# Performance work log

Measured on AMD Instinct MI355X. Metric: run time of the kernel, lower is better.

Reference implementation:

```python
import jax, jax.numpy as jnp
import numpy as np

# Standard SMPL kinematic tree (24 joints)
PARENTS = np.array([-1, 0, 0, 0, 1, 2, 3, 4, 5, 6, 7, 8, 9, 9, 9, 12, 13, 14, 16, 17, 18, 19, 20, 21], dtype=np.int32)
B, V, J, NB = 1024, 6890, 24, 10  # batch, vertices, joints, betas


def _rodrigues(r):
    """Axis-angle (..., 3) -> rotation matrices (..., 3, 3)."""
    theta = jnp.sqrt(jnp.sum(r * r, axis=-1, keepdims=True) + 1e-8)
    axis = r / theta
    c = jnp.cos(theta)[..., None]
    s = jnp.sin(theta)[..., None]
    x, y, z = axis[..., 0], axis[..., 1], axis[..., 2]
    zeros = jnp.zeros_like(x)
    K = jnp.stack([zeros, -z, y, z, zeros, -x, -y, x, zeros], axis=-1).reshape(r.shape[:-1] + (3, 3))
    outer = axis[..., :, None] * axis[..., None, :]
    eye = jnp.eye(3, dtype=r.dtype)
    return c * eye + (1.0 - c) * outer + s * K


def setup_inputs() -> dict:
    key = jax.random.key(0)
    ks = jax.random.split(key, 9)
    shape = jax.random.normal(ks[0], (B, NB), dtype=jnp.float32)
    body_pose = jax.random.normal(ks[1], (B, J - 1, 3), dtype=jnp.float32) * 0.2
    pelvis_rotation = jax.random.normal(ks[2], (B, 3), dtype=jnp.float32) * 0.2
    global_translation = jax.random.normal(ks[3], (B, 3), dtype=jnp.float32)
    v_template = jax.random.normal(ks[4], (V, 3), dtype=jnp.float32) * 0.3
    shapedirs = jax.random.normal(ks[5], (V, 3, NB), dtype=jnp.float32) * 0.01
    posedirs = jax.random.normal(ks[6], ((J - 1) * 9, V * 3), dtype=jnp.float32) * 0.01
    lbs_weights = jax.nn.softmax(jax.random.normal(ks[7], (V, J), dtype=jnp.float32) * 4.0, axis=-1)
    J_regressor = jax.nn.softmax(jax.random.normal(ks[8], (J, V), dtype=jnp.float32) * 4.0, axis=-1)
    parents = jnp.asarray(PARENTS)
    return {"shape": shape, "body_pose": body_pose, "pelvis_rotation": pelvis_rotation,
            "global_translation": global_translation, "v_template": v_template,
            "shapedirs": shapedirs, "posedirs": posedirs, "lbs_weights": lbs_weights,
            "J_regressor": J_regressor, "parents": parents}


def reference(shape, body_pose, pelvis_rotation, global_translation,
              v_template, shapedirs, posedirs, lbs_weights, J_regressor, parents):
    b = shape.shape[0]
    dtype = shape.dtype
    # --- shape blendshapes ---
    v_shaped = v_template + jnp.einsum('bl,vcl->bvc', shape, shapedirs)        # (B, V, 3)
    joints = jnp.einsum('jv,bvc->bjc', J_regressor, v_shaped)                  # (B, J, 3)
    # --- pose rotations + pose blendshapes ---
    full_pose = jnp.concatenate([pelvis_rotation[:, None, :], body_pose], axis=1)  # (B, J, 3)
    rot = _rodrigues(full_pose)                                                # (B, J, 3, 3)
    pose_feat = (rot[:, 1:] - jnp.eye(3, dtype=dtype)).reshape(b, (J - 1) * 9)
    v_posed = v_shaped + (pose_feat @ posedirs).reshape(b, -1, 3)              # (B, V, 3)
    # --- forward kinematics along tree ---
    rel_joints = joints.at[:, 1:].add(-joints[:, PARENTS[1:]])                 # (B, J, 3)
    T = jnp.concatenate([rot, rel_joints[..., None]], axis=-1)                 # (B, J, 3, 4)
    bottom = jnp.broadcast_to(jnp.asarray([0, 0, 0, 1], dtype=dtype), (b, J, 1, 4))
    T = jnp.concatenate([T, bottom], axis=-2)                                  # (B, J, 4, 4)
    chain = [T[:, 0]]
    for j in range(1, J):
        chain.append(chain[int(PARENTS[j])] @ T[:, j])
    A = jnp.stack(chain, axis=1)                                               # (B, J, 4, 4)
    # --- remove rest-pose joint locations ---
    t_corr = A[..., :3, 3] - jnp.einsum('bjxy,bjy->bjx', A[..., :3, :3], joints)
    A_rel = A.at[..., :3, 3].set(t_corr)
    # --- linear blend skinning ---
    Tv = jnp.einsum('vj,bjxy->bvxy', lbs_weights, A_rel)                       # (B, V, 4, 4)
    verts = jnp.einsum('bvxy,bvy->bvx', Tv[..., :3, :3], v_posed) + Tv[..., :3, 3]
    return verts + global_translation[:, None, :]                              # (B, V, 3)
```

## Files before the change

kernel.cpp:

```cpp
#include <hip/hip_runtime.h>
#include <stdint.h>

#define V_   6890
#define N3   20670
#define NPAD 20736
#define VPAD 7168
#define J_   24
#define NB_  10
#define KP   207
#define KE   224
#define LDP  201

typedef __attribute__((ext_vector_type(8))) short bf16x8;
typedef __attribute__((ext_vector_type(4))) float f32x4;

__device__ __forceinline__ float bf2f(ushort u) {
    union { uint32_t u; float f; } cv; cv.u = ((uint32_t)u) << 16; return cv.f;
}
__device__ __forceinline__ ushort f2bf(float f) {
    union { float f; uint32_t u; } cv; cv.f = f;
    uint32_t u = cv.u;
    u += 0x7FFFu + ((u >> 16) & 1u);
    return (ushort)(u >> 16);
}

__global__ __launch_bounds__(256) void k_jreg(const float* __restrict__ jreg,
                                              const float* __restrict__ vt,
                                              const float* __restrict__ sd,
                                              float* __restrict__ jsp) {
    int j = blockIdx.x, c = blockIdx.y;
    int t = threadIdx.x;
    float acc[33];
#pragma unroll
    for (int i = 0; i < 33; i++) acc[i] = 0.f;
#pragma unroll
    for (int it = 0; it < 2; it++) {
        int v = c * 512 + it * 256 + t;
        if (v < V_) {
            float w = jreg[(size_t)j * V_ + v];
            acc[0] += w * vt[v * 3 + 0];
            acc[1] += w * vt[v * 3 + 1];
            acc[2] += w * vt[v * 3 + 2];
            const float* sdv = sd + (size_t)v * 30;
#pragma unroll
            for (int i = 0; i < 30; i++) acc[3 + i] += w * sdv[i];
        }
    }
    __shared__ float red[256][33];
#pragma unroll
    for (int i = 0; i < 33; i++) red[t][i] = acc[i];
    __syncthreads();
    for (int s = 128; s > 0; s >>= 1) {
        if (t < s) {
#pragma unroll
            for (int i = 0; i < 33; i++) red[t][i] += red[t + s][i];
        }
        __syncthreads();
    }
    if (t < 33) jsp[(size_t)(j * 14 + c) * 33 + t] = red[0][t];
}

__global__ __launch_bounds__(832) void k_jred(const float* __restrict__ jsp,
                                              float* __restrict__ js) {
    int t = threadIdx.x;
    if (t >= 792) return;
    int j = t / 33, i = t % 33;
    float s = 0.f;
#pragma unroll
    for (int c = 0; c < 14; c++) s += jsp[(size_t)(j * 14 + c) * 33 + i];
    js[t] = s;
}

__global__ __launch_bounds__(256) void k_bext(const float* __restrict__ pd,
                                              const float* __restrict__ sd,
                                              const float* __restrict__ vt,
                                              ushort* __restrict__ bt) {
    int n  = blockIdx.x * 256 + threadIdx.x;
    int k0 = blockIdx.y * 8;
    bool valid = n < N3;
    union { ushort s[8]; uint4 v; } u;
#pragma unroll
    for (int i = 0; i < 8; i++) {
        int k = k0 + i;
        float x = 0.f;
        if (valid) {
            if (k < KP)              x = pd[(size_t)k * N3 + n];
            else if (k < KP + NB_)   x = sd[(size_t)n * NB_ + (k - KP)];
            else if (k == KP + NB_)  x = vt[n];
        }
        u.s[i] = f2bf(x);
    }
    *(uint4*)(bt + (size_t)n * KE + k0) = u.v;
}

__global__ __launch_bounds__(256) void k_wbf(const float* __restrict__ lw,
                                             ushort* __restrict__ w_hi,
                                             ushort* __restrict__ w_lo) {
    int i = blockIdx.x * 256 + threadIdx.x;
    int v = i >> 5, j = i & 31;
    float x = (j < 24 && v < V_) ? lw[(size_t)v * 24 + j] : 0.f;
    ushort hi = f2bf(x);
    w_hi[i] = hi;
    w_lo[i] = f2bf(x - bf2f(hi));
}

__global__ __launch_bounds__(64) void k_pose(const float* __restrict__ shape,
                                             const float* __restrict__ body_pose,
                                             const float* __restrict__ pelvis,
                                             const float* __restrict__ js,
                                             ushort* __restrict__ pfext,
                                             ushort* __restrict__ aT_hi,
                                             ushort* __restrict__ aT_lo,
                                             int Breal) {
    int b = blockIdx.x;
    int t = threadIdx.x;
    if (b >= Breal) {
        uint32_t* pz = (uint32_t*)(pfext + (size_t)b * KE);
        for (int i = t; i < KE / 2; i += 64) pz[i] = 0;
        return;
    }
    __shared__ float Rs[24][9];
    __shared__ float Js[24][3];
    __shared__ float As[24][12];

    if (t < 24) {
        float rx, ry, rz;
        if (t == 0) {
            rx = pelvis[b * 3 + 0]; ry = pelvis[b * 3 + 1]; rz = pelvis[b * 3 + 2];
        } else {
            const float* p = body_pose + ((size_t)b * 23 + (t - 1)) * 3;
            rx = p[0]; ry = p[1]; rz = p[2];
        }
        float th = sqrtf(rx * rx + ry * ry + rz * rz + 1e-8f);
        float inv = 1.f / th;
        float x = rx * inv, y = ry * inv, z = rz * inv;
        float c = cosf(th), s = sinf(th), omc = 1.f - c;
        float R[9];
        R[0] = c + omc * x * x;     R[1] = omc * x * y - s * z; R[2] = omc * x * z + s * y;
        R[3] = omc * y * x + s * z; R[4] = c + omc * y * y;     R[5] = omc * y * z - s * x;
        R[6] = omc * z * x - s * y; R[7] = omc * z * y + s * x; R[8] = c + omc * z * z;
#pragma unroll
        for (int e = 0; e < 9; e++) Rs[t][e] = R[e];

        const float* jsj = js + t * 33;
        float sh[10];
#pragma unroll
        for (int l = 0; l < 10; l++) sh[l] = shape[b * 10 + l];
#pragma unroll
        for (int c2 = 0; c2 < 3; c2++) {
            float a = jsj[c2];
#pragma unroll
            for (int l = 0; l < 10; l++) a += sh[l] * jsj[3 + c2 * 10 + l];
            Js[t][c2] = a;
        }
        ushort* pf = pfext + (size_t)b * KE;
        if (t >= 1) {
#pragma unroll
            for (int e = 0; e < 9; e++) {
                float v = R[e] - ((e == 0 || e == 4 || e == 8) ? 1.f : 0.f);
                pf[(t - 1) * 9 + e] = f2bf(v);
            }
        } else {
            for (int l = 0; l < 10; l++) pf[KP + l] = f2bf(sh[l]);
            pf[KP + NB_] = 0x3F80;
            for (int k = KP + NB_ + 1; k < KE; k++) pf[k] = 0;
        }
    }
    __syncthreads();

    if (t < 12) {
        int row = t >> 2, col = t & 3;
        As[0][t] = (col < 3) ? Rs[0][row * 3 + col] : Js[0][row];
    }
    __syncthreads();
    const int par[24] = {-1,0,0,0,1,2,3,4,5,6,7,8,9,9,9,12,13,14,16,17,18,19,20,21};
#pragma unroll 1
    for (int j = 1; j < 24; j++) {
        int p = par[j];
        float val = 0.f;
        if (t < 12) {
            int row = t >> 2, col = t & 3;
            if (col < 3) {
                val = As[p][row * 4 + 0] * Rs[j][0 * 3 + col]
                    + As[p][row * 4 + 1] * Rs[j][1 * 3 + col]
                    + As[p][row * 4 + 2] * Rs[j][2 * 3 + col];
            } else {
                float relx = Js[j][0] - Js[p][0];
                float rely = Js[j][1] - Js[p][1];
                float relz = Js[j][2] - Js[p][2];
                val = As[p][row * 4 + 0] * relx + As[p][row * 4 + 1] * rely
                    + As[p][row * 4 + 2] * relz + As[p][row * 4 + 3];
            }
        }
        __syncthreads();
        if (t < 12) As[j][t] = val;
        __syncthreads();
    }
    if (t < 24) {
        float tc[3];
#pragma unroll
        for (int row = 0; row < 3; row++) {
            float r0 = As[t][row * 4 + 0], r1 = As[t][row * 4 + 1], r2 = As[t][row * 4 + 2];
            tc[row] = As[t][row * 4 + 3] - (r0 * Js[t][0] + r1 * Js[t][1] + r2 * Js[t][2]);
        }
        As[t][3] = tc[0]; As[t][7] = tc[1]; As[t][11] = tc[2];
    }
    __syncthreads();
    ushort* dh = aT_hi + (size_t)b * 512;
    ushort* dl = aT_lo + (size_t)b * 512;
    for (int i = t; i < 512; i += 64) {
        int e = i >> 5, j = i & 31;
        float val = (e < 12 && j < 24) ? As[j][e] : 0.f;
        ushort hi = f2bf(val);
        dh[i] = hi;
        dl[i] = f2bf(val - bf2f(hi));
    }
}

__global__ __launch_bounds__(256) void k_fused(const ushort* __restrict__ bt,
                                               const ushort* __restrict__ pfext,
                                               const ushort* __restrict__ aT_hi,
                                               const ushort* __restrict__ aT_lo,
                                               const ushort* __restrict__ w_hi,
                                               const ushort* __restrict__ w_lo,
                                               const float* __restrict__ trans,
                                               float* __restrict__ vert,
                                               int Breal) {
    int lane = threadIdx.x & 63;
    int wv   = threadIdx.x >> 6;
    int quad = lane >> 4;
    int m    = lane & 15;
    int vtile = blockIdx.x;
    int nbase = vtile * 192;
    int bbase = blockIdx.y * 64 + wv * 16;

    __shared__ float posed[64][LDP];

    f32x4 acc[12];
#pragma unroll
    for (int f = 0; f < 12; f++) acc[f] = (f32x4){0.f, 0.f, 0.f, 0.f};

    const ushort* bp = pfext + (size_t)(bbase + m) * KE + quad * 8;
    const ushort* ap = bt + (size_t)(nbase + m) * KE + quad * 8;
#pragma unroll 2
    for (int ks = 0; ks < 7; ks++) {
        bf16x8 bfrag = *(const bf16x8*)(bp + ks * 32);
#pragma unroll
        for (int f = 0; f < 12; f++) {
            bf16x8 afrag = *(const bf16x8*)(ap + (size_t)(f * 16) * KE + ks * 32);
            acc[f] = __builtin_amdgcn_mfma_f32_16x16x32_bf16(afrag, bfrag, acc[f], 0, 0, 0);
        }
    }
    {
        float* dst0 = &posed[wv * 16 + m][quad * 4];
#pragma unroll
        for (int f = 0; f < 12; f++) {
            float* dst = dst0 + f * 16;
            dst[0] = acc[f][0]; dst[1] = acc[f][1]; dst[2] = acc[f][2]; dst[3] = acc[f][3];
        }
    }
    __syncthreads();

    bf16x8 Wh[4], Wl[4];
#pragma unroll
    for (int i = 0; i < 4; i++) {
        size_t offw = (size_t)((vtile * 4 + i) * 16 + m) * 32 + quad * 8;
        Wh[i] = *(const bf16x8*)(w_hi + offw);
        Wl[i] = *(const bf16x8*)(w_lo + offw);
    }

#pragma unroll 1
    for (int bb = 0; bb < 16; bb++) {
        int b = bbase + bb;
        if (b >= Breal) break;
        size_t aoff = (size_t)b * 512 + m * 32 + quad * 8;
        bf16x8 Ah = *(const bf16x8*)(aT_hi + aoff);
        bf16x8 Al = *(const bf16x8*)(aT_lo + aoff);
        float tq = (quad < 3) ? trans[b * 3 + quad] : 0.f;
        const float* pr = &posed[wv * 16 + bb][0];
        float* vrow = vert + (size_t)b * N3;
#pragma unroll
        for (int i = 0; i < 4; i++) {
            int vloc = i * 16 + m;
            int v = vtile * 64 + vloc;
            float p0 = pr[vloc * 3 + 0];
            float p1 = pr[vloc * 3 + 1];
            float p2 = pr[vloc * 3 + 2];
            f32x4 a2 = (f32x4){0.f, 0.f, 0.f, 0.f};
            a2 = __builtin_amdgcn_mfma_f32_16x16x32_bf16(Ah, Wh[i], a2, 0, 0, 0);
            a2 = __builtin_amdgcn_mfma_f32_16x16x32_bf16(Al, Wh[i], a2, 0, 0, 0);
            a2 = __builtin_amdgcn_mfma_f32_16x16x32_bf16(Ah, Wl[i], a2, 0, 0, 0);
            float res = a2[0] * p0 + a2[1] * p1 + a2[2] * p2 + a2[3] + tq;
            if (quad < 3 && v < V_)
                vrow[3 * v + quad] = res;
        }
    }
}

extern "C" void kernel_launch(void* const* d_in, const int* in_sizes, int n_in,
                              void* d_out, int out_size, void* d_ws, size_t ws_size,
                              hipStream_t stream) {
    const float* shape = (const float*)d_in[0];
    const float* bpose = (const float*)d_in[1];
    const float* pelv  = (const float*)d_in[2];
    const float* trans = (const float*)d_in[3];
    const float* vt    = (const float*)d_in[4];
    const float* sd    = (const float*)d_in[5];
    const float* pd    = (const float*)d_in[6];
    const float* lw    = (const float*)d_in[7];
    const float* jr    = (const float*)d_in[8];
    float* out = (float*)d_out;

    int B    = in_sizes[0] / NB_;
    int Bpad = (B + 63) & ~63;

    char* ws = (char*)d_ws;
    size_t off = 0;
    auto alloc = [&](size_t bytes) { char* p = ws + off; off += (bytes + 255) & ~(size_t)255; return p; };
    float*  jsp   = (float*) alloc(24 * 14 * 33 * 4);
    float*  js    = (float*) alloc(24 * 33 * 4);
    ushort* pfext = (ushort*)alloc((size_t)Bpad * KE * 2);
    ushort* aT_hi = (ushort*)alloc((size_t)B * 512 * 2);
    ushort* aT_lo = (ushort*)alloc((size_t)B * 512 * 2);
    ushort* w_hi  = (ushort*)alloc((size_t)VPAD * 32 * 2);
    ushort* w_lo  = (ushort*)alloc((size_t)VPAD * 32 * 2);
    ushort* bt    = (ushort*)alloc((size_t)NPAD * KE * 2);

    k_jreg<<<dim3(24, 14), 256, 0, stream>>>(jr, vt, sd, jsp);
    k_jred<<<1, 832, 0, stream>>>(jsp, js);
    k_bext<<<dim3(NPAD / 256, KE / 8), 256, 0, stream>>>(pd, sd, vt, bt);
    k_wbf<<<VPAD * 32 / 256, 256, 0, stream>>>(lw, w_hi, w_lo);
    k_pose<<<Bpad, 64, 0, stream>>>(shape, bpose, pelv, js, pfext, aT_hi, aT_lo, B);
    k_fused<<<dim3(NPAD / 192, Bpad / 64), 256, 0, stream>>>(bt, pfext, aT_hi, aT_lo,
                                                             w_hi, w_lo, trans, out, B);
}
```

Measured before the change: 217.1 us.

## Retile fused skinning kernel to 32-batch blocks with XCD swizzle and prefetch

The fused GEMM+skinning kernel now uses a 1D grid of 32-batch by 192-column tiles. The four waves split into two batch halves by two column halves, so each wave only reads the posed values it wrote, which replaces __syncthreads with an LDS waitcnt. A block-index swizzle spreads consecutive tiles across the 8 XCDs, the per-batch transform fragments are prefetched one iteration ahead, and the LDS row pitch is padded to allow aligned vector stores. The change doubles the number of blocks and halves accumulator registers, at the cost of loading pfext rows twice as often per column tile.

```diff
diff --git a/kernel.cpp b/kernel.cpp
--- a/kernel.cpp
+++ b/kernel.cpp
@@ -9,7 +9,7 @@
 #define NB_  10
 #define KP   207
 #define KE   224
-#define LDP  201
+#define LDP  204
 
 typedef __attribute__((ext_vector_type(8))) short bf16x8;
 typedef __attribute__((ext_vector_type(4))) float f32x4;
@@ -225,67 +225,78 @@
                                                const ushort* __restrict__ w_lo,
                                                const float* __restrict__ trans,
                                                float* __restrict__ vert,
-                                               int Breal) {
+                                               int Breal, int NY) {
     int lane = threadIdx.x & 63;
     int wv   = threadIdx.x >> 6;
     int quad = lane >> 4;
     int m    = lane & 15;
-    int vtile = blockIdx.x;
-    int nbase = vtile * 192;
-    int bbase = blockIdx.y * 64 + wv * 16;
-
-    __shared__ float posed[64][LDP];
-
-    f32x4 acc[12];
-#pragma unroll
-    for (int f = 0; f < 12; f++) acc[f] = (f32x4){0.f, 0.f, 0.f, 0.f};
-
-    const ushort* bp = pfext + (size_t)(bbase + m) * KE + quad * 8;
-    const ushort* ap = bt + (size_t)(nbase + m) * KE + quad * 8;
+    int bh   = wv & 1;
+    int nh   = wv >> 1;
+
+    int bid = blockIdx.x;
+    int cpx = (108 * NY) >> 3;
+    int sw  = (bid & 7) * cpx + (bid >> 3);
+    unsigned uNY = (unsigned)NY;
+    int vtile = (int)((unsigned)sw / uNY);
+    int by    = sw - vtile * NY;
+
+    int nbase_w = vtile * 192 + nh * 96;
+    int bbase_w = by * 32 + bh * 16;
+
+    __shared__ __align__(16) float posed[32][LDP];
+
+    bf16x8 Wh[2], Wl[2];
+#pragma unroll
+    for (int i = 0; i < 2; i++) {
+        size_t offw = (size_t)((vtile * 4 + nh * 2 + i) * 16 + m) * 32 + quad * 8;
+        Wh[i] = *(const bf16x8*)(w_hi + offw);
+        Wl[i] = *(const bf16x8*)(w_lo + offw);
+    }
+
+    f32x4 acc[6];
+#pragma unroll
+    for (int f = 0; f < 6; f++) acc[f] = (f32x4){0.f, 0.f, 0.f, 0.f};
+
+    const ushort* bp = pfext + (size_t)(bbase_w + m) * KE + quad * 8;
+    const ushort* ap = bt + (size_t)(nbase_w + m) * KE + quad * 8;
 #pragma unroll 2
     for (int ks = 0; ks < 7; ks++) {
         bf16x8 bfrag = *(const bf16x8*)(bp + ks * 32);
 #pragma unroll
-        for (int f = 0; f < 12; f++) {
+        for (int f = 0; f < 6; f++) {
             bf16x8 afrag = *(const bf16x8*)(ap + (size_t)(f * 16) * KE + ks * 32);
             acc[f] = __builtin_amdgcn_mfma_f32_16x16x32_bf16(afrag, bfrag, acc[f], 0, 0, 0);
         }
     }
-    {
-        float* dst0 = &posed[wv * 16 + m][quad * 4];
-#pragma unroll
-        for (int f = 0; f < 12; f++) {
-            float* dst = dst0 + f * 16;
-            dst[0] = acc[f][0]; dst[1] = acc[f][1]; dst[2] = acc[f][2]; dst[3] = acc[f][3];
-        }
-    }
-    __syncthreads();
-
-    bf16x8 Wh[4], Wl[4];
-#pragma unroll
-    for (int i = 0; i < 4; i++) {
-        size_t offw = (size_t)((vtile * 4 + i) * 16 + m) * 32 + quad * 8;
-        Wh[i] = *(const bf16x8*)(w_hi + offw);
-        Wl[i] = *(const bf16x8*)(w_lo + offw);
-    }
+#pragma unroll
+    for (int f = 0; f < 6; f++)
+        *(f32x4*)&posed[bh * 16 + m][nh * 96 + f * 16 + quad * 4] = acc[f];
+
+    __asm volatile("s_waitcnt lgkmcnt(0)" ::: "memory");
+
+    int col0 = nh * 96 + 3 * m;
+    size_t aoff0 = (size_t)bbase_w * 512 + m * 32 + quad * 8;
+    bf16x8 Ah = *(const bf16x8*)(aT_hi + aoff0);
+    bf16x8 Al = *(const bf16x8*)(aT_lo + aoff0);
 
 #pragma unroll 1
     for (int bb = 0; bb < 16; bb++) {
-        int b = bbase + bb;
+        int b = bbase_w + bb;
         if (b >= Breal) break;
-        size_t aoff = (size_t)b * 512 + m * 32 + quad * 8;
-        bf16x8 Ah = *(const bf16x8*)(aT_hi + aoff);
-        bf16x8 Al = *(const bf16x8*)(aT_lo + aoff);
+        int bn = (bb < 15 && b + 1 < Breal) ? b + 1 : b;
+        size_t aoffn = (size_t)bn * 512 + m * 32 + quad * 8;
+        bf16x8 Ah_n = *(const bf16x8*)(aT_hi + aoffn);
+        bf16x8 Al_n = *(const bf16x8*)(aT_lo + aoffn);
         float tq = (quad < 3) ? trans[b * 3 + quad] : 0.f;
-        const float* pr = &posed[wv * 16 + bb][0];
+        const float* pr = &posed[bh * 16 + bb][0];
         float* vrow = vert + (size_t)b * N3;
 #pragma unroll
-        for (int i = 0; i < 4; i++) {
-            int vloc = i * 16 + m;
+        for (int i = 0; i < 2; i++) {
+            int vloc = nh * 32 + i * 16 + m;
             int v = vtile * 64 + vloc;
-            float p0 = pr[vloc * 3 + 0];
-            float p1 = pr[vloc * 3 + 1];
-            float p2 = pr[vloc * 3 + 2];
+            float p0 = pr[col0 + i * 48 + 0];
+            float p1 = pr[col0 + i * 48 + 1];
+            float p2 = pr[col0 + i * 48 + 2];
             f32x4 a2 = (f32x4){0.f, 0.f, 0.f, 0.f};
             a2 = __builtin_amdgcn_mfma_f32_16x16x32_bf16(Ah, Wh[i], a2, 0, 0, 0);
             a2 = __builtin_amdgcn_mfma_f32_16x16x32_bf16(Al, Wh[i], a2, 0, 0, 0);
@@ -294,6 +305,7 @@
             if (quad < 3 && v < V_)
                 vrow[3 * v + quad] = res;
         }
+        Ah = Ah_n; Al = Al_n;
     }
 }
 
@@ -313,6 +325,7 @@
 
     int B    = in_sizes[0] / NB_;
     int Bpad = (B + 63) & ~63;
+    int NY   = Bpad / 32;
 
     char* ws = (char*)d_ws;
     size_t off = 0;
@@ -331,6 +344,6 @@
     k_bext<<<dim3(NPAD / 256, KE / 8), 256, 0, stream>>>(pd, sd, vt, bt);
     k_wbf<<<VPAD * 32 / 256, 256, 0, stream>>>(lw, w_hi, w_lo);
     k_pose<<<Bpad, 64, 0, stream>>>(shape, bpose, pelv, js, pfext, aT_hi, aT_lo, B);
-    k_fused<<<dim3(NPAD / 192, Bpad / 64), 256, 0, stream>>>(bt, pfext, aT_hi, aT_lo,
-                                                             w_hi, w_lo, trans, out, B);
-}
+    k_fused<<<dim3(108 * NY), 256, 0, stream>>>(bt, pfext, aT_hi, aT_lo,
+                                                w_hi, w_lo, trans, out, B, NY);
+}
```

Result: slower. 227.3 us (+4.7%).

## Merge prep kernels, swizzle fused grid, pipeline skinning epilogue two batches at a time

Applied to the files above, without the earlier changes.

Merges the blendshape-matrix and weight conversion kernels into one launch, and folds the joint partial-sum reduction into the pose kernel, removing two launches. The fused kernel now uses a 1D grid remapped so that neighbouring blocks are spread across XCDs, which is meant to improve cache locality. The block-wide barrier is replaced by a wave-local LDS wait, since each wave reads only its own rows of the posed tile. The posed tile is padded and stored with vector writes, and the skinning epilogue handles two batches per iteration while prefetching the next transform fragments. The cost is higher register pressure, and the reduction work is repeated redundantly in every pose block.

```diff
diff --git a/kernel.cpp b/kernel.cpp
--- a/kernel.cpp
+++ b/kernel.cpp
@@ -9,7 +9,7 @@
 #define NB_  10
 #define KP   207
 #define KE   224
-#define LDP  201
+#define LDP  204
 
 typedef __attribute__((ext_vector_type(8))) short bf16x8;
 typedef __attribute__((ext_vector_type(4))) float f32x4;
@@ -60,54 +60,47 @@
     if (t < 33) jsp[(size_t)(j * 14 + c) * 33 + t] = red[0][t];
 }
 
-__global__ __launch_bounds__(832) void k_jred(const float* __restrict__ jsp,
-                                              float* __restrict__ js) {
-    int t = threadIdx.x;
-    if (t >= 792) return;
-    int j = t / 33, i = t % 33;
-    float s = 0.f;
-#pragma unroll
-    for (int c = 0; c < 14; c++) s += jsp[(size_t)(j * 14 + c) * 33 + i];
-    js[t] = s;
-}
-
-__global__ __launch_bounds__(256) void k_bext(const float* __restrict__ pd,
+__global__ __launch_bounds__(256) void k_prep(const float* __restrict__ pd,
                                               const float* __restrict__ sd,
                                               const float* __restrict__ vt,
-                                              ushort* __restrict__ bt) {
-    int n  = blockIdx.x * 256 + threadIdx.x;
-    int k0 = blockIdx.y * 8;
-    bool valid = n < N3;
-    union { ushort s[8]; uint4 v; } u;
-#pragma unroll
-    for (int i = 0; i < 8; i++) {
-        int k = k0 + i;
-        float x = 0.f;
-        if (valid) {
-            if (k < KP)              x = pd[(size_t)k * N3 + n];
-            else if (k < KP + NB_)   x = sd[(size_t)n * NB_ + (k - KP)];
-            else if (k == KP + NB_)  x = vt[n];
-        }
-        u.s[i] = f2bf(x);
-    }
-    *(uint4*)(bt + (size_t)n * KE + k0) = u.v;
-}
-
-__global__ __launch_bounds__(256) void k_wbf(const float* __restrict__ lw,
-                                             ushort* __restrict__ w_hi,
-                                             ushort* __restrict__ w_lo) {
-    int i = blockIdx.x * 256 + threadIdx.x;
-    int v = i >> 5, j = i & 31;
-    float x = (j < 24 && v < V_) ? lw[(size_t)v * 24 + j] : 0.f;
-    ushort hi = f2bf(x);
-    w_hi[i] = hi;
-    w_lo[i] = f2bf(x - bf2f(hi));
+                                              const float* __restrict__ lw,
+                                              ushort* __restrict__ bt,
+                                              ushort* __restrict__ w_hi,
+                                              ushort* __restrict__ w_lo) {
+    int g = blockIdx.x;
+    int t = threadIdx.x;
+    if (g < 81 * 28) {
+        int nblk = g % 81, kblk = g / 81;
+        int n  = nblk * 256 + t;
+        int k0 = kblk * 8;
+        bool valid = n < N3;
+        union { ushort s[8]; uint4 v; } u;
+#pragma unroll
+        for (int i = 0; i < 8; i++) {
+            int k = k0 + i;
+            float x = 0.f;
+            if (valid) {
+                if (k < KP)              x = pd[(size_t)k * N3 + n];
+                else if (k < KP + NB_)   x = sd[(size_t)n * NB_ + (k - KP)];
+                else if (k == KP + NB_)  x = vt[n];
+            }
+            u.s[i] = f2bf(x);
+        }
+        *(uint4*)(bt + (size_t)n * KE + k0) = u.v;
+    } else {
+        int i = (g - 81 * 28) * 256 + t;
+        int v = i >> 5, j = i & 31;
+        float x = (j < 24 && v < V_) ? lw[(size_t)v * 24 + j] : 0.f;
+        ushort hi = f2bf(x);
+        w_hi[i] = hi;
+        w_lo[i] = f2bf(x - bf2f(hi));
+    }
 }
 
 __global__ __launch_bounds__(64) void k_pose(const float* __restrict__ shape,
                                              const float* __restrict__ body_pose,
                                              const float* __restrict__ pelvis,
-                                             const float* __restrict__ js,
+                                             const float* __restrict__ jsp,
                                              ushort* __restrict__ pfext,
                                              ushort* __restrict__ aT_hi,
                                              ushort* __restrict__ aT_lo,
@@ -119,9 +112,19 @@
         for (int i = t; i < KE / 2; i += 64) pz[i] = 0;
         return;
     }
+    __shared__ float js_s[792];
     __shared__ float Rs[24][9];
     __shared__ float Js[24][3];
     __shared__ float As[24][12];
+
+    for (int idx = t; idx < 792; idx += 64) {
+        int j = idx / 33, i = idx - j * 33;
+        float s = 0.f;
+#pragma unroll
+        for (int c = 0; c < 14; c++) s += jsp[(size_t)(j * 14 + c) * 33 + i];
+        js_s[idx] = s;
+    }
+    __syncthreads();
 
     if (t < 24) {
         float rx, ry, rz;
@@ -142,7 +145,7 @@
 #pragma unroll
         for (int e = 0; e < 9; e++) Rs[t][e] = R[e];
 
-        const float* jsj = js + t * 33;
+        const float* jsj = js_s + t * 33;
         float sh[10];
 #pragma unroll
         for (int l = 0; l < 10; l++) sh[l] = shape[b * 10 + l];
@@ -225,22 +228,37 @@
                                                const ushort* __restrict__ w_lo,
                                                const float* __restrict__ trans,
                                                float* __restrict__ vert,
-                                               int Breal) {
+                                               int Breal, int NYB) {
     int lane = threadIdx.x & 63;
     int wv   = threadIdx.x >> 6;
     int quad = lane >> 4;
     int m    = lane & 15;
-    int vtile = blockIdx.x;
-    int nbase = vtile * 192;
-    int bbase = blockIdx.y * 64 + wv * 16;
-
-    __shared__ float posed[64][LDP];
+
+    int bid = blockIdx.x;
+    int cpx = (108 * NYB) >> 3;
+    int sw  = (bid & 7) * cpx + (bid >> 3);
+    unsigned uNYB = (unsigned)NYB;
+    int vtile = (int)((unsigned)sw / uNYB);
+    int by    = sw - vtile * NYB;
+
+    int nbase   = vtile * 192;
+    int bbase_w = by * 64 + wv * 16;
+
+    __shared__ __align__(16) float posed[64][LDP];
+
+    bf16x8 Wh[4], Wl[4];
+#pragma unroll
+    for (int i = 0; i < 4; i++) {
+        size_t offw = (size_t)((vtile * 4 + i) * 16 + m) * 32 + quad * 8;
+        Wh[i] = *(const bf16x8*)(w_hi + offw);
+        Wl[i] = *(const bf16x8*)(w_lo + offw);
+    }
 
     f32x4 acc[12];
 #pragma unroll
     for (int f = 0; f < 12; f++) acc[f] = (f32x4){0.f, 0.f, 0.f, 0.f};
 
-    const ushort* bp = pfext + (size_t)(bbase + m) * KE + quad * 8;
+    const ushort* bp = pfext + (size_t)(bbase_w + m) * KE + quad * 8;
     const ushort* ap = bt + (size_t)(nbase + m) * KE + quad * 8;
 #pragma unroll 2
     for (int ks = 0; ks < 7; ks++) {
@@ -251,49 +269,65 @@
             acc[f] = __builtin_amdgcn_mfma_f32_16x16x32_bf16(afrag, bfrag, acc[f], 0, 0, 0);
         }
     }
-    {
-        float* dst0 = &posed[wv * 16 + m][quad * 4];
-#pragma unroll
-        for (int f = 0; f < 12; f++) {
-            float* dst = dst0 + f * 16;
-            dst[0] = acc[f][0]; dst[1] = acc[f][1]; dst[2] = acc[f][2]; dst[3] = acc[f][3];
-        }
-    }
-    __syncthreads();
-
-    bf16x8 Wh[4], Wl[4];
-#pragma unroll
-    for (int i = 0; i < 4; i++) {
-        size_t offw = (size_t)((vtile * 4 + i) * 16 + m) * 32 + quad * 8;
-        Wh[i] = *(const bf16x8*)(w_hi + offw);
-        Wl[i] = *(const bf16x8*)(w_lo + offw);
-    }
+#pragma unroll
+    for (int f = 0; f < 12; f++)
+        *(f32x4*)&posed[wv * 16 + m][f * 16 + quad * 4] = acc[f];
+
+    __asm volatile("s_waitcnt lgkmcnt(0)" ::: "memory");
+
+    size_t fragoff = (size_t)m * 32 + quad * 8;
+    auto aoff = [&](int bb) {
+        int b = bbase_w + bb;
+        if (b >= Breal) b = Breal - 1;
+        return (size_t)b * 512 + fragoff;
+    };
+
+    bf16x8 Ah0 = *(const bf16x8*)(aT_hi + aoff(0));
+    bf16x8 Al0 = *(const bf16x8*)(aT_lo + aoff(0));
+    bf16x8 Ah1 = *(const bf16x8*)(aT_hi + aoff(1));
+    bf16x8 Al1 = *(const bf16x8*)(aT_lo + aoff(1));
 
 #pragma unroll 1
-    for (int bb = 0; bb < 16; bb++) {
-        int b = bbase + bb;
-        if (b >= Breal) break;
-        size_t aoff = (size_t)b * 512 + m * 32 + quad * 8;
-        bf16x8 Ah = *(const bf16x8*)(aT_hi + aoff);
-        bf16x8 Al = *(const bf16x8*)(aT_lo + aoff);
-        float tq = (quad < 3) ? trans[b * 3 + quad] : 0.f;
-        const float* pr = &posed[wv * 16 + bb][0];
-        float* vrow = vert + (size_t)b * N3;
+    for (int bb = 0; bb < 16; bb += 2) {
+        int pf = (bb + 2 < 16) ? bb + 2 : bb;
+        bf16x8 AhN0 = *(const bf16x8*)(aT_hi + aoff(pf));
+        bf16x8 AlN0 = *(const bf16x8*)(aT_lo + aoff(pf));
+        bf16x8 AhN1 = *(const bf16x8*)(aT_hi + aoff(pf + 1));
+        bf16x8 AlN1 = *(const bf16x8*)(aT_lo + aoff(pf + 1));
+
+        int b0 = bbase_w + bb, b1 = b0 + 1;
+        float tq0 = 0.f, tq1 = 0.f;
+        if (quad < 3) {
+            if (b0 < Breal) tq0 = trans[b0 * 3 + quad];
+            if (b1 < Breal) tq1 = trans[b1 * 3 + quad];
+        }
+        const float* pr0 = &posed[wv * 16 + bb][0];
+        const float* pr1 = &posed[wv * 16 + bb + 1][0];
+        float* vrow0 = vert + (size_t)b0 * N3;
+        float* vrow1 = vert + (size_t)b1 * N3;
 #pragma unroll
         for (int i = 0; i < 4; i++) {
             int vloc = i * 16 + m;
             int v = vtile * 64 + vloc;
-            float p0 = pr[vloc * 3 + 0];
-            float p1 = pr[vloc * 3 + 1];
-            float p2 = pr[vloc * 3 + 2];
-            f32x4 a2 = (f32x4){0.f, 0.f, 0.f, 0.f};
-            a2 = __builtin_amdgcn_mfma_f32_16x16x32_bf16(Ah, Wh[i], a2, 0, 0, 0);
-            a2 = __builtin_amdgcn_mfma_f32_16x16x32_bf16(Al, Wh[i], a2, 0, 0, 0);
-            a2 = __builtin_amdgcn_mfma_f32_16x16x32_bf16(Ah, Wl[i], a2, 0, 0, 0);
-            float res = a2[0] * p0 + a2[1] * p1 + a2[2] * p2 + a2[3] + tq;
-            if (quad < 3 && v < V_)
-                vrow[3 * v + quad] = res;
-        }
+            int c0 = vloc * 3;
+            float p00 = pr0[c0], p01 = pr0[c0 + 1], p02 = pr0[c0 + 2];
+            float p10 = pr1[c0], p11 = pr1[c0 + 1], p12 = pr1[c0 + 2];
+            f32x4 a20 = (f32x4){0.f, 0.f, 0.f, 0.f};
+            f32x4 a21 = (f32x4){0.f, 0.f, 0.f, 0.f};
+            a20 = __builtin_amdgcn_mfma_f32_16x16x32_bf16(Ah0, Wh[i], a20, 0, 0, 0);
+            a21 = __builtin_amdgcn_mfma_f32_16x16x32_bf16(Ah1, Wh[i], a21, 0, 0, 0);
+            a20 = __builtin_amdgcn_mfma_f32_16x16x32_bf16(Al0, Wh[i], a20, 0, 0, 0);
+            a21 = __builtin_amdgcn_mfma_f32_16x16x32_bf16(Al1, Wh[i], a21, 0, 0, 0);
+            a20 = __builtin_amdgcn_mfma_f32_16x16x32_bf16(Ah0, Wl[i], a20, 0, 0, 0);
+            a21 = __builtin_amdgcn_mfma_f32_16x16x32_bf16(Ah1, Wl[i], a21, 0, 0, 0);
+            float res0 = a20[0] * p00 + a20[1] * p01 + a20[2] * p02 + a20[3] + tq0;
+            float res1 = a21[0] * p10 + a21[1] * p11 + a21[2] * p12 + a21[3] + tq1;
+            if (quad < 3 && v < V_) {
+                if (b0 < Breal) vrow0[3 * v + quad] = res0;
+                if (b1 < Breal) vrow1[3 * v + quad] = res1;
+            }
+        }
+        Ah0 = AhN0; Al0 = AlN0; Ah1 = AhN1; Al1 = AlN1;
     }
 }
 
@@ -313,12 +347,12 @@
 
     int B    = in_sizes[0] / NB_;
     int Bpad = (B + 63) & ~63;
+    int NYB  = Bpad / 64;
 
     char* ws = (char*)d_ws;
     size_t off = 0;
     auto alloc = [&](size_t bytes) { char* p = ws + off; off += (bytes + 255) & ~(size_t)255; return p; };
     float*  jsp   = (float*) alloc(24 * 14 * 33 * 4);
-    float*  js    = (float*) alloc(24 * 33 * 4);
     ushort* pfext = (ushort*)alloc((size_t)Bpad * KE * 2);
     ushort* aT_hi = (ushort*)alloc((size_t)B * 512 * 2);
     ushort* aT_lo = (ushort*)alloc((size_t)B * 512 * 2);
@@ -327,10 +361,8 @@
     ushort* bt    = (ushort*)alloc((size_t)NPAD * KE * 2);
 
     k_jreg<<<dim3(24, 14), 256, 0, stream>>>(jr, vt, sd, jsp);
-    k_jred<<<1, 832, 0, stream>>>(jsp, js);
-    k_bext<<<dim3(NPAD / 256, KE / 8), 256, 0, stream>>>(pd, sd, vt, bt);
-    k_wbf<<<VPAD * 32 / 256, 256, 0, stream>>>(lw, w_hi, w_lo);
-    k_pose<<<Bpad, 64, 0, stream>>>(shape, bpose, pelv, js, pfext, aT_hi, aT_lo, B);
-    k_fused<<<dim3(NPAD / 192, Bpad / 64), 256, 0, stream>>>(bt, pfext, aT_hi, aT_lo,
-                                                             w_hi, w_lo, trans, out, B);
-}
+    k_prep<<<81 * 28 + VPAD * 32 / 256, 256, 0, stream>>>(pd, sd, vt, lw, bt, w_hi, w_lo);
+    k_pose<<<Bpad, 64, 0, stream>>>(shape, bpose, pelv, jsp, pfext, aT_hi, aT_lo, B);
+    k_fused<<<dim3(108 * NYB), 256, 0, stream>>>(bt, pfext, aT_hi, aT_lo,
+                                                 w_hi, w_lo, trans, out, B, NYB);
+}
```

After: 225.9 us. +4.1%, slower.

## Fuse preprocessing kernels into one launch and retile posed GEMM per wave

Applied to the files above, without the earlier changes.

Merges the joint-regressor partial sums, posedirs/shapedirs bf16 packing, and LBS-weight hi/lo split into a single kernel dispatched by block index. The final joint reduction moves into k_pose, where each block recomputes it into shared memory, so the single-block reduction launch disappears. The shared-memory reduction is chunked into 11-wide pieces to cut LDS use. In the fused GEMM, each wave now computes 48 vertices × 64 batches (3×4 MFMA tiles) instead of 192 × 16, so A fragments are reused across batch tiles. The cost is redundant reduction work in every pose block and different register and load pressure in the GEMM.

```diff
diff --git a/kernel.cpp b/kernel.cpp
--- a/kernel.cpp
+++ b/kernel.cpp
@@ -24,90 +24,84 @@
     return (ushort)(u >> 16);
 }
 
-__global__ __launch_bounds__(256) void k_jreg(const float* __restrict__ jreg,
-                                              const float* __restrict__ vt,
-                                              const float* __restrict__ sd,
-                                              float* __restrict__ jsp) {
-    int j = blockIdx.x, c = blockIdx.y;
-    int t = threadIdx.x;
-    float acc[33];
-#pragma unroll
-    for (int i = 0; i < 33; i++) acc[i] = 0.f;
-#pragma unroll
-    for (int it = 0; it < 2; it++) {
-        int v = c * 512 + it * 256 + t;
-        if (v < V_) {
-            float w = jreg[(size_t)j * V_ + v];
-            acc[0] += w * vt[v * 3 + 0];
-            acc[1] += w * vt[v * 3 + 1];
-            acc[2] += w * vt[v * 3 + 2];
-            const float* sdv = sd + (size_t)v * 30;
-#pragma unroll
-            for (int i = 0; i < 30; i++) acc[3 + i] += w * sdv[i];
-        }
-    }
-    __shared__ float red[256][33];
-#pragma unroll
-    for (int i = 0; i < 33; i++) red[t][i] = acc[i];
-    __syncthreads();
-    for (int s = 128; s > 0; s >>= 1) {
-        if (t < s) {
-#pragma unroll
-            for (int i = 0; i < 33; i++) red[t][i] += red[t + s][i];
-        }
-        __syncthreads();
-    }
-    if (t < 33) jsp[(size_t)(j * 14 + c) * 33 + t] = red[0][t];
-}
-
-__global__ __launch_bounds__(832) void k_jred(const float* __restrict__ jsp,
-                                              float* __restrict__ js) {
-    int t = threadIdx.x;
-    if (t >= 792) return;
-    int j = t / 33, i = t % 33;
-    float s = 0.f;
-#pragma unroll
-    for (int c = 0; c < 14; c++) s += jsp[(size_t)(j * 14 + c) * 33 + i];
-    js[t] = s;
-}
-
-__global__ __launch_bounds__(256) void k_bext(const float* __restrict__ pd,
-                                              const float* __restrict__ sd,
-                                              const float* __restrict__ vt,
-                                              ushort* __restrict__ bt) {
-    int n  = blockIdx.x * 256 + threadIdx.x;
-    int k0 = blockIdx.y * 8;
-    bool valid = n < N3;
-    union { ushort s[8]; uint4 v; } u;
-#pragma unroll
-    for (int i = 0; i < 8; i++) {
-        int k = k0 + i;
-        float x = 0.f;
-        if (valid) {
-            if (k < KP)              x = pd[(size_t)k * N3 + n];
-            else if (k < KP + NB_)   x = sd[(size_t)n * NB_ + (k - KP)];
-            else if (k == KP + NB_)  x = vt[n];
-        }
-        u.s[i] = f2bf(x);
-    }
-    *(uint4*)(bt + (size_t)n * KE + k0) = u.v;
-}
-
-__global__ __launch_bounds__(256) void k_wbf(const float* __restrict__ lw,
+__global__ __launch_bounds__(256) void k_pre(const float* __restrict__ jreg,
+                                             const float* __restrict__ vt,
+                                             const float* __restrict__ sd,
+                                             const float* __restrict__ pd,
+                                             const float* __restrict__ lw,
+                                             float* __restrict__ jsp,
+                                             ushort* __restrict__ bt,
                                              ushort* __restrict__ w_hi,
                                              ushort* __restrict__ w_lo) {
-    int i = blockIdx.x * 256 + threadIdx.x;
-    int v = i >> 5, j = i & 31;
-    float x = (j < 24 && v < V_) ? lw[(size_t)v * 24 + j] : 0.f;
-    ushort hi = f2bf(x);
-    w_hi[i] = hi;
-    w_lo[i] = f2bf(x - bf2f(hi));
+    int g = blockIdx.x;
+    int t = threadIdx.x;
+    if (g < 336) {
+        int j = g % 24, c = g / 24;
+        float acc[33];
+#pragma unroll
+        for (int i = 0; i < 33; i++) acc[i] = 0.f;
+#pragma unroll
+        for (int it = 0; it < 2; it++) {
+            int v = c * 512 + it * 256 + t;
+            if (v < V_) {
+                float w = jreg[(size_t)j * V_ + v];
+                acc[0] += w * vt[v * 3 + 0];
+                acc[1] += w * vt[v * 3 + 1];
+                acc[2] += w * vt[v * 3 + 2];
+                const float* sdv = sd + (size_t)v * 30;
+#pragma unroll
+                for (int i = 0; i < 30; i++) acc[3 + i] += w * sdv[i];
+            }
+        }
+        __shared__ float red[256][11];
+#pragma unroll 1
+        for (int ch = 0; ch < 3; ch++) {
+#pragma unroll
+            for (int i = 0; i < 11; i++) red[t][i] = acc[ch * 11 + i];
+            __syncthreads();
+            for (int s = 128; s > 0; s >>= 1) {
+                if (t < s) {
+#pragma unroll
+                    for (int i = 0; i < 11; i++) red[t][i] += red[t + s][i];
+                }
+                __syncthreads();
+            }
+            if (t < 11) jsp[(size_t)(j * 14 + c) * 33 + ch * 11 + t] = red[0][t];
+            __syncthreads();
+        }
+    } else if (g < 336 + 81 * 28) {
+        int gg = g - 336;
+        int nblk = gg % 81, kblk = gg / 81;
+        int n  = nblk * 256 + t;
+        int k0 = kblk * 8;
+        bool valid = n < N3;
+        union { ushort s[8]; uint4 v; } u;
+#pragma unroll
+        for (int i = 0; i < 8; i++) {
+            int k = k0 + i;
+            float x = 0.f;
+            if (valid) {
+                if (k < KP)              x = pd[(size_t)k * N3 + n];
+                else if (k < KP + NB_)   x = sd[(size_t)n * NB_ + (k - KP)];
+                else if (k == KP + NB_)  x = vt[n];
+            }
+            u.s[i] = f2bf(x);
+        }
+        *(uint4*)(bt + (size_t)n * KE + k0) = u.v;
+    } else {
+        int i = (g - 336 - 81 * 28) * 256 + t;
+        int v = i >> 5, j = i & 31;
+        float x = (j < 24 && v < V_) ? lw[(size_t)v * 24 + j] : 0.f;
+        ushort hi = f2bf(x);
+        w_hi[i] = hi;
+        w_lo[i] = f2bf(x - bf2f(hi));
+    }
 }
 
 __global__ __launch_bounds__(64) void k_pose(const float* __restrict__ shape,
                                              const float* __restrict__ body_pose,
                                              const float* __restrict__ pelvis,
-                                             const float* __restrict__ js,
+                                             const float* __restrict__ jsp,
                                              ushort* __restrict__ pfext,
                                              ushort* __restrict__ aT_hi,
                                              ushort* __restrict__ aT_lo,
@@ -119,9 +113,19 @@
         for (int i = t; i < KE / 2; i += 64) pz[i] = 0;
         return;
     }
+    __shared__ float js_s[792];
     __shared__ float Rs[24][9];
     __shared__ float Js[24][3];
     __shared__ float As[24][12];
+
+    for (int idx = t; idx < 792; idx += 64) {
+        int j = idx / 33, i = idx - j * 33;
+        float s = 0.f;
+#pragma unroll
+        for (int c = 0; c < 14; c++) s += jsp[(size_t)(j * 14 + c) * 33 + i];
+        js_s[idx] = s;
+    }
+    __syncthreads();
 
     if (t < 24) {
         float rx, ry, rz;
@@ -142,7 +146,7 @@
 #pragma unroll
         for (int e = 0; e < 9; e++) Rs[t][e] = R[e];
 
-        const float* jsj = js + t * 33;
+        const float* jsj = js_s + t * 33;
         float sh[10];
 #pragma unroll
         for (int l = 0; l < 10; l++) sh[l] = shape[b * 10 + l];
@@ -232,33 +236,42 @@
     int m    = lane & 15;
     int vtile = blockIdx.x;
     int nbase = vtile * 192;
-    int bbase = blockIdx.y * 64 + wv * 16;
+    int bblk  = blockIdx.y * 64;
+    int bbase = bblk + wv * 16;
 
     __shared__ float posed[64][LDP];
 
-    f32x4 acc[12];
-#pragma unroll
-    for (int f = 0; f < 12; f++) acc[f] = (f32x4){0.f, 0.f, 0.f, 0.f};
-
-    const ushort* bp = pfext + (size_t)(bbase + m) * KE + quad * 8;
-    const ushort* ap = bt + (size_t)(nbase + m) * KE + quad * 8;
+    f32x4 acc[3][4];
+#pragma unroll
+    for (int f = 0; f < 3; f++)
+#pragma unroll
+        for (int gq = 0; gq < 4; gq++) acc[f][gq] = (f32x4){0.f, 0.f, 0.f, 0.f};
+
+    const ushort* ap = bt + (size_t)(nbase + wv * 48 + m) * KE + quad * 8;
+    const ushort* bp = pfext + (size_t)(bblk + m) * KE + quad * 8;
 #pragma unroll 2
     for (int ks = 0; ks < 7; ks++) {
-        bf16x8 bfrag = *(const bf16x8*)(bp + ks * 32);
-#pragma unroll
-        for (int f = 0; f < 12; f++) {
-            bf16x8 afrag = *(const bf16x8*)(ap + (size_t)(f * 16) * KE + ks * 32);
-            acc[f] = __builtin_amdgcn_mfma_f32_16x16x32_bf16(afrag, bfrag, acc[f], 0, 0, 0);
-        }
-    }
-    {
-        float* dst0 = &posed[wv * 16 + m][quad * 4];
-#pragma unroll
-        for (int f = 0; f < 12; f++) {
-            float* dst = dst0 + f * 16;
-            dst[0] = acc[f][0]; dst[1] = acc[f][1]; dst[2] = acc[f][2]; dst[3] = acc[f][3];
-        }
-    }
+        bf16x8 av[3], bv[4];
+#pragma unroll
+        for (int f = 0; f < 3; f++)
+            av[f] = *(const bf16x8*)(ap + (size_t)(f * 16) * KE + ks * 32);
+#pragma unroll
+        for (int gq = 0; gq < 4; gq++)
+            bv[gq] = *(const bf16x8*)(bp + (size_t)(gq * 16) * KE + ks * 32);
+#pragma unroll
+        for (int f = 0; f < 3; f++)
+#pragma unroll
+            for (int gq = 0; gq < 4; gq++)
+                acc[f][gq] = __builtin_amdgcn_mfma_f32_16x16x32_bf16(av[f], bv[gq], acc[f][gq], 0, 0, 0);
+    }
+#pragma unroll
+    for (int f = 0; f < 3; f++)
+#pragma unroll
+        for (int gq = 0; gq < 4; gq++) {
+            float* dst = &posed[gq * 16 + m][wv * 48 + f * 16 + quad * 4];
+            dst[0] = acc[f][gq][0]; dst[1] = acc[f][gq][1];
+            dst[2] = acc[f][gq][2]; dst[3] = acc[f][gq][3];
+        }
     __syncthreads();
 
     bf16x8 Wh[4], Wl[4];
@@ -318,7 +331,6 @@
     size_t off = 0;
     auto alloc = [&](size_t bytes) { char* p = ws + off; off += (bytes + 255) & ~(size_t)255; return p; };
     float*  jsp   = (float*) alloc(24 * 14 * 33 * 4);
-    float*  js    = (float*) alloc(24 * 33 * 4);
     ushort* pfext = (ushort*)alloc((size_t)Bpad * KE * 2);
     ushort* aT_hi = (ushort*)alloc((size_t)B * 512 * 2);
     ushort* aT_lo = (ushort*)alloc((size_t)B * 512 * 2);
@@ -326,11 +338,9 @@
     ushort* w_lo  = (ushort*)alloc((size_t)VPAD * 32 * 2);
     ushort* bt    = (ushort*)alloc((size_t)NPAD * KE * 2);
 
-    k_jreg<<<dim3(24, 14), 256, 0, stream>>>(jr, vt, sd, jsp);
-    k_jred<<<1, 832, 0, stream>>>(jsp, js);
-    k_bext<<<dim3(NPAD / 256, KE / 8), 256, 0, stream>>>(pd, sd, vt, bt);
-    k_wbf<<<VPAD * 32 / 256, 256, 0, stream>>>(lw, w_hi, w_lo);
-    k_pose<<<Bpad, 64, 0, stream>>>(shape, bpose, pelv, js, pfext, aT_hi, aT_lo, B);
-    k_fused<<<dim3(NPAD / 192, Bpad / 64), 256, 0, stream>>>(bt, pfext, aT_hi, aT_lo,
-                                                             w_hi, w_lo, trans, out, B);
-}
+    k_pre<<<336 + 81 * 28 + VPAD * 32 / 256, 256, 0, stream>>>(jr, vt, sd, pd, lw,
+                                                               jsp, bt, w_hi, w_lo);
+    k_pose<<<Bpad, 64, 0, stream>>>(shape, bpose, pelv, jsp, pfext, aT_hi, aT_lo, B);
+    k_fused<<<dim3(108, Bpad / 64), 256, 0, stream>>>(bt, pfext, aT_hi, aT_lo,
+                                                      w_hi, w_lo, trans, out, B);
+}
```

New measurement: 207.7 us. 1.05x faster.
